# Kernel tuning notes

Measured on AMD Instinct MI355X. Metric: run time of the kernel, lower is better.

Reference implementation:

```python
import jax, jax.numpy as jnp
import numpy as np

B, S, H, NH, L = 2, 1024, 512, 8, 4
HD = H // NH
MLP = 4 * H
OUT = 128
SPARSITY = 0.8
EPS = 1e-5


def _pos_encoding(seq_len, d_model):
    pos = jnp.arange(seq_len, dtype=jnp.float32)[:, None]                     # [S,1]
    div = jnp.exp(jnp.arange(0, d_model, 2, dtype=jnp.float32) * (-np.log(10000.0) / d_model))
    ang = pos * div                                                            # [S,D/2]
    pe = jnp.stack([jnp.sin(ang), jnp.cos(ang)], axis=-1).reshape(seq_len, d_model)
    return pe[None]                                                            # [1,S,D]


def _layer_norm(x, g, b):
    m = jnp.mean(x, axis=-1, keepdims=True)
    v = jnp.mean(jnp.square(x - m), axis=-1, keepdims=True)
    return (x - m) * jax.lax.rsqrt(v + EPS) * g + b


def setup_inputs() -> dict:
    key = jax.random.key(0)
    ks = iter(jax.random.split(key, 16))
    w = lambda k, shp: jax.random.normal(k, shp, dtype=jnp.float32) * 0.02
    inp = {
        "x": jax.random.normal(next(ks), (B, S), dtype=jnp.float32),
        "in_w": w(next(ks), (1, H)), "in_b": jnp.zeros((H,), jnp.float32),
        "ln1_g": jnp.ones((L, H), jnp.float32), "ln1_b": jnp.zeros((L, H), jnp.float32),
        "qw": w(next(ks), (L, H, H)), "qb": jnp.zeros((L, H), jnp.float32),
        "kw": w(next(ks), (L, H, H)), "kb": jnp.zeros((L, H), jnp.float32),
        "vw": w(next(ks), (L, H, H)), "vb": jnp.zeros((L, H), jnp.float32),
        "ow": w(next(ks), (L, H, H)), "ob": jnp.zeros((L, H), jnp.float32),
        "ln2_g": jnp.ones((L, H), jnp.float32), "ln2_b": jnp.zeros((L, H), jnp.float32),
        "w1": w(next(ks), (L, H, MLP)), "b1": jnp.zeros((L, MLP), jnp.float32),
        "w2": w(next(ks), (L, MLP, H)), "b2": jnp.zeros((L, H), jnp.float32),
        "fn_g": jnp.ones((H,), jnp.float32), "fn_b": jnp.zeros((H,), jnp.float32),
        "out_w": w(next(ks), (H, OUT)), "out_b": jnp.zeros((OUT,), jnp.float32),
    }
    return inp


def _forward(x, in_w, in_b, ln1_g, ln1_b, qw, qb, kw, kb, vw, vb, ow, ob,
             ln2_g, ln2_b, w1, b1, w2, b2, fn_g, fn_b, out_w, out_b):
    seq_len = x.shape[1]
    k_top = max(1, int(seq_len * (1.0 - SPARSITY)))  # static
    scale = HD ** -0.5

    h = x[..., None] @ in_w + in_b                    # [B,S,H] (input_proj on [B,S,1])
    h = h + _pos_encoding(seq_len, H)

    layer_params = (ln1_g, ln1_b, qw, qb, kw, kb, vw, vb, ow, ob,
                    ln2_g, ln2_b, w1, b1, w2, b2)

    def block(h, p):
        (g1, bb1, Wq, bq, Wk, bk, Wv, bv, Wo, bo, g2, bb2, W1, B1, W2, B2) = p
        n = _layer_norm(h, g1, bb1)
        # project and split heads: [B,S,H] -> [B,NH,S,HD]
        def heads(W, b):
            y = n @ W + b
            return y.reshape(B, seq_len, NH, HD).transpose(0, 2, 1, 3)
        q, k, v = heads(Wq, bq), heads(Wk, bk), heads(Wv, bv)
        scores = jnp.einsum('bhqd,bhkd->bhqk', q, k) * scale
        # top-k sparsification: keep entries >= k-th largest per row (-inf elsewhere)
        kth = jax.lax.top_k(scores, k_top)[0][..., -1:]
        sparse = jnp.where(scores >= kth, scores, -jnp.inf)
        attn = jax.nn.softmax(sparse, axis=-1)
        o = jnp.einsum('bhqk,bhkd->bhqd', attn, v)
        o = o.transpose(0, 2, 1, 3).reshape(B, seq_len, H)
        h = h + (o @ Wo + bo)
        m = _layer_norm(h, g2, bb2)
        m = jax.nn.gelu(m @ W1 + B1, approximate=False) @ W2 + B2
        return h + m, attn

    h, attn_stack = jax.lax.scan(block, h, layer_params)
    out = _layer_norm(h, fn_g, fn_b) @ out_w + out_b  # [B,S,OUT]
    return out, attn_stack                            # attn_stack: [L,B,NH,S,S]


def reference(x, in_w, in_b, ln1_g, ln1_b, qw, qb, kw, kb, vw, vb, ow, ob,
              ln2_g, ln2_b, w1, b1, w2, b2, fn_g, fn_b, out_w, out_b):
    return _forward(x, in_w, in_b, ln1_g, ln1_b, qw, qb, kw, kb, vw, vb, ow, ob,
                    ln2_g, ln2_b, w1, b1, w2, b2, fn_g, fn_b, out_w, out_b)
```

## Files before the change

kernel.cpp:

```cpp
#include <hip/hip_runtime.h>
#include <math.h>

#define DEVINL __device__ __forceinline__

constexpr int S_   = 1024;
constexpr int H_   = 512;
constexpr int NH_  = 8;
constexpr int L_   = 4;
constexpr int HD_  = 64;
constexpr int MLP_ = 2048;
constexpr int OUT_ = 128;
constexpr int B_   = 2;
constexpr int BS_  = 2048;
constexpr int KTOP_ = 204;

typedef __bf16 bf16x8 __attribute__((ext_vector_type(8)));
typedef float f32x4 __attribute__((ext_vector_type(4)));

DEVINL unsigned short f2b(float f) {
  unsigned int u = __float_as_uint(f);
  unsigned int r = (u + 0x7fffu + ((u >> 16) & 1u)) >> 16;
  return (unsigned short)r;
}

__global__ __launch_bounds__(256) void transpose_conv_kernel(
    const float* __restrict__ src, unsigned short* __restrict__ dst, int R, int C)
{
  __shared__ float tile[32][33];
  const size_t base = (size_t)blockIdx.z * R * C;
  src += base; dst += base;
  const int c0 = blockIdx.x * 32;
  const int r0 = blockIdx.y * 32;
  const int tx = threadIdx.x & 31;
  const int ty = threadIdx.x >> 5;
#pragma unroll
  for (int j = 0; j < 4; j++)
    tile[ty + j * 8][tx] = src[(size_t)(r0 + ty + j * 8) * C + c0 + tx];
  __syncthreads();
#pragma unroll
  for (int j = 0; j < 4; j++)
    dst[(size_t)(c0 + ty + j * 8) * R + r0 + tx] = f2b(tile[tx][ty + j * 8]);
}

__global__ __launch_bounds__(256) void transpose_qkvo_kernel(
    const float* __restrict__ qw, const float* __restrict__ kw,
    const float* __restrict__ vw, const float* __restrict__ ow,
    unsigned short* __restrict__ qkv, unsigned short* __restrict__ ot)
{
  __shared__ float tile[32][33];
  const int z = blockIdx.z;
  const int which = z >> 2, l = z & 3;
  const float* src = (which == 0 ? qw : which == 1 ? kw : which == 2 ? vw : ow)
                     + (size_t)l * 512 * 512;
  unsigned short* dst = (which < 3)
      ? (qkv + (size_t)l * 1536 * 512 + (size_t)which * 512 * 512)
      : (ot + (size_t)l * 512 * 512);
  const int c0 = blockIdx.x * 32;
  const int r0 = blockIdx.y * 32;
  const int tx = threadIdx.x & 31;
  const int ty = threadIdx.x >> 5;
#pragma unroll
  for (int j = 0; j < 4; j++)
    tile[ty + j * 8][tx] = src[(size_t)(r0 + ty + j * 8) * 512 + c0 + tx];
  __syncthreads();
#pragma unroll
  for (int j = 0; j < 4; j++)
    dst[(size_t)(c0 + ty + j * 8) * 512 + r0 + tx] = f2b(tile[tx][ty + j * 8]);
}

__global__ __launch_bounds__(128) void input_pe_kernel(
    const float* __restrict__ x, const float* __restrict__ in_w,
    const float* __restrict__ in_b, float* __restrict__ h)
{
  const int row = blockIdx.x;
  const int s = row & (S_ - 1);
  const int c = threadIdx.x * 4;
  const float xv = x[row];
  const float4 wv = *(const float4*)(in_w + c);
  const float4 bv = *(const float4*)(in_b + c);
  const float* wp = (const float*)&wv;
  const float* bp = (const float*)&bv;
  float o[4];
#pragma unroll
  for (int j = 0; j < 4; j++) {
    const int cc = c + j;
    const float di = expf(-(float)(cc & ~1) * (9.210340371976184f / 512.0f));
    const float ang = (float)s * di;
    const float pe = (cc & 1) ? cosf(ang) : sinf(ang);
    o[j] = xv * wp[j] + bp[j] + pe;
  }
  *(float4*)(h + (size_t)row * H_ + c) = make_float4(o[0], o[1], o[2], o[3]);
}

__global__ __launch_bounds__(128) void ln_kernel(
    const float* __restrict__ hin, const float* __restrict__ g,
    const float* __restrict__ b, unsigned short* __restrict__ nout)
{
  const int row = blockIdx.x;
  const int t = threadIdx.x;
  const int wid = t >> 6, ln_ = t & 63;
  __shared__ float red[2];
  float4 v = ((const float4*)(hin + (size_t)row * H_))[t];
  float sm = v.x + v.y + v.z + v.w;
#pragma unroll
  for (int m = 1; m < 64; m <<= 1) sm += __shfl_xor(sm, m);
  if (ln_ == 0) red[wid] = sm;
  __syncthreads();
  const float mean = (red[0] + red[1]) * (1.0f / 512.0f);
  __syncthreads();
  const float dx = v.x - mean, dy = v.y - mean, dz = v.z - mean, dw = v.w - mean;
  float ss = dx * dx + dy * dy + dz * dz + dw * dw;
#pragma unroll
  for (int m = 1; m < 64; m <<= 1) ss += __shfl_xor(ss, m);
  if (ln_ == 0) red[wid] = ss;
  __syncthreads();
  const float var = (red[0] + red[1]) * (1.0f / 512.0f);
  const float rs = rsqrtf(var + 1e-5f);
  const float4 gv = ((const float4*)g)[t];
  const float4 bv = ((const float4*)b)[t];
  ushort4 o;
  o.x = f2b(dx * rs * gv.x + bv.x);
  o.y = f2b(dy * rs * gv.y + bv.y);
  o.z = f2b(dz * rs * gv.z + bv.z);
  o.w = f2b(dw * rs * gv.w + bv.w);
  ((ushort4*)(nout + (size_t)row * H_))[t] = o;
}

template <int EPI>
__global__ __launch_bounds__(256, 2) void gemm_kernel(
    const unsigned short* __restrict__ A, const unsigned short* __restrict__ Bt,
    const float* __restrict__ bias, void* __restrict__ Cout, int M, int N, int K,
    const float* __restrict__ bias2, const float* __restrict__ bias3,
    void* __restrict__ C2, void* __restrict__ C3)
{
  constexpr int LDK = 56;
  __shared__ unsigned short Alds[128 * LDK];
  __shared__ unsigned short Blds[128 * LDK];
  const int tid = threadIdx.x;
  const int w = tid >> 6, lane = tid & 63, lr = lane & 15, lg = lane >> 4;
  const int m0 = blockIdx.x * 128, n0 = blockIdx.y * 128;
  const int wm = (w >> 1) * 64, wn = (w & 1) * 64;

  const int e0 = tid * 8;
  const int r0 = e0 >> 5, c0 = e0 & 31;
  const unsigned short* Ap0 = A + (size_t)(m0 + r0) * K + c0;
  const unsigned short* Ap1 = Ap0 + (size_t)64 * K;
  const unsigned short* Bp0 = Bt + (size_t)(n0 + r0) * K + c0;
  const unsigned short* Bp1 = Bp0 + (size_t)64 * K;
  unsigned short* AL0 = Alds + r0 * LDK + c0;
  unsigned short* AL1 = AL0 + 64 * LDK;
  unsigned short* BL0 = Blds + r0 * LDK + c0;
  unsigned short* BL1 = BL0 + 64 * LDK;

  const f32x4 zero4 = {0.f, 0.f, 0.f, 0.f};
  f32x4 acc[4][4];
#pragma unroll
  for (int i = 0; i < 4; i++)
#pragma unroll
    for (int j = 0; j < 4; j++) acc[i][j] = zero4;

  for (int kt = 0; kt < K; kt += 32) {
    const int4 a0 = *(const int4*)(Ap0 + kt);
    const int4 a1 = *(const int4*)(Ap1 + kt);
    const int4 b0 = *(const int4*)(Bp0 + kt);
    const int4 b1 = *(const int4*)(Bp1 + kt);
    __syncthreads();
    *(int4*)AL0 = a0; *(int4*)AL1 = a1;
    *(int4*)BL0 = b0; *(int4*)BL1 = b1;
    __syncthreads();
    bf16x8 af[4], bfr[4];
#pragma unroll
    for (int mi = 0; mi < 4; mi++)
      af[mi] = *(const bf16x8*)(Alds + (wm + mi * 16 + lr) * LDK + lg * 8);
#pragma unroll
    for (int ni = 0; ni < 4; ni++)
      bfr[ni] = *(const bf16x8*)(Blds + (wn + ni * 16 + lr) * LDK + lg * 8);
#pragma unroll
    for (int mi = 0; mi < 4; mi++)
#pragma unroll
      for (int ni = 0; ni < 4; ni++)
        acc[mi][ni] = __builtin_amdgcn_mfma_f32_16x16x32_bf16(af[mi], bfr[ni], acc[mi][ni], 0, 0, 0);
  }

#pragma unroll
  for (int mi = 0; mi < 4; mi++) {
#pragma unroll
    for (int ni = 0; ni < 4; ni++) {
      const int col = n0 + wn + ni * 16 + lr;
      if constexpr (EPI == 5) {
        if (col < 512) {
          const float bs = bias[col];
#pragma unroll
          for (int r = 0; r < 4; r++) {
            const int row = m0 + wm + mi * 16 + lg * 4 + r;
            ((unsigned short*)Cout)[(size_t)row * 512 + col] =
                f2b((acc[mi][ni][r] + bs) * 0.125f);
          }
        } else if (col < 1024) {
          const float bs = bias2[col - 512];
#pragma unroll
          for (int r = 0; r < 4; r++) {
            const int row = m0 + wm + mi * 16 + lg * 4 + r;
            ((unsigned short*)C2)[(size_t)row * 512 + (col - 512)] =
                f2b(acc[mi][ni][r] + bs);
          }
        } else {
          const float bs = bias3[col - 1024];
          const int row0_ = m0 + wm + mi * 16 + lg * 4;
          const int bb = row0_ >> 10, ssi = row0_ & 1023;
          ushort4 pk;
          pk.x = f2b(acc[mi][ni][0] + bs);
          pk.y = f2b(acc[mi][ni][1] + bs);
          pk.z = f2b(acc[mi][ni][2] + bs);
          pk.w = f2b(acc[mi][ni][3] + bs);
          *(ushort4*)((unsigned short*)C3 + ((size_t)(bb * 512 + (col - 1024))) * 1024 + ssi) = pk;
        }
      } else {
        const float bs = bias[col];
#pragma unroll
        for (int r = 0; r < 4; r++) {
          const int row = m0 + wm + mi * 16 + lg * 4 + r;
          float val = acc[mi][ni][r] + bs;
          const size_t idx = (size_t)row * N + col;
          if constexpr (EPI == 1) {
            ((float*)Cout)[idx] += val;
          } else if constexpr (EPI == 2) {
            val = 0.5f * val * (1.0f + erff(val * 0.7071067811865475f));
            ((unsigned short*)Cout)[idx] = f2b(val);
          } else {
            ((float*)Cout)[idx] = val;
          }
        }
      }
    }
  }
}

__global__ __launch_bounds__(256, 2) void attn_fused_kernel(
    const unsigned short* __restrict__ qbf, const unsigned short* __restrict__ kbf,
    const unsigned short* __restrict__ vt, float* __restrict__ attnL,
    unsigned short* __restrict__ obf)
{
  constexpr int LDF = 1032;
  __shared__ float sc[16 * LDF];
  const int mblk = blockIdx.x, bnh = blockIdx.y;
  const int b = bnh >> 3, nh = bnh & 7;
  const int tid = threadIdx.x, w = tid >> 6, lane = tid & 63;
  const int lr = lane & 15, lg = lane >> 4;
  const int row0 = mblk * 16;

  const unsigned short* qbase = qbf + ((size_t)(b * S_ + row0)) * H_ + nh * HD_;
  const unsigned short* kbase = kbf + (size_t)(b * S_) * H_ + nh * HD_;

  const f32x4 zero4 = {0.f, 0.f, 0.f, 0.f};

  {
    f32x4 acc[16];
#pragma unroll
    for (int kt = 0; kt < 16; kt++) acc[kt] = zero4;
    bf16x8 qf[2];
    qf[0] = *(const bf16x8*)(qbase + (size_t)lr * H_ + lg * 8);
    qf[1] = *(const bf16x8*)(qbase + (size_t)lr * H_ + 32 + lg * 8);
    const int kw0 = w * 256;
#pragma unroll
    for (int kt = 0; kt < 16; kt++) {
      const unsigned short* kp = kbase + (size_t)(kw0 + kt * 16 + lr) * H_ + lg * 8;
      const bf16x8 kf0 = *(const bf16x8*)(kp);
      const bf16x8 kf1 = *(const bf16x8*)(kp + 32);
      acc[kt] = __builtin_amdgcn_mfma_f32_16x16x32_bf16(kf0, qf[0], acc[kt], 0, 0, 0);
      acc[kt] = __builtin_amdgcn_mfma_f32_16x16x32_bf16(kf1, qf[1], acc[kt], 0, 0, 0);
    }
#pragma unroll
    for (int kt = 0; kt < 16; kt++)
      *(f32x4*)(sc + (size_t)lr * LDF + kw0 + kt * 16 + lg * 4) = acc[kt];
  }
  __syncthreads();

#pragma unroll 1
  for (int rr = 0; rr < 4; rr++) {
    const int row = w * 4 + rr;
    float* rowp = sc + (size_t)row * LDF;
    float v[16];
#pragma unroll
    for (int j = 0; j < 8; j++) {
      const float2 t2 = *(const float2*)(rowp + 2 * lane + j * 128);
      v[2 * j] = t2.x; v[2 * j + 1] = t2.y;
    }
    unsigned int keys[16];
#pragma unroll
    for (int j = 0; j < 16; j++) {
      const unsigned int u = __float_as_uint(v[j]);
      keys[j] = (u & 0x80000000u) ? ~u : (u | 0x80000000u);
    }
    unsigned int prefix = 0u;
#pragma unroll 1
    for (int bit = 31; bit >= 0; bit--) {
      const unsigned int cand = prefix | (1u << bit);
      int cnt = 0;
#pragma unroll
      for (int j = 0; j < 16; j++)
        cnt += (int)__popcll(__ballot(keys[j] >= cand));
      if (cnt >= KTOP_) prefix = cand;
    }
    const unsigned int fb = (prefix & 0x80000000u) ? (prefix & 0x7fffffffu) : ~prefix;
    const float thresh = __uint_as_float(fb);

    float mx = v[0];
#pragma unroll
    for (int j = 1; j < 16; j++) mx = fmaxf(mx, v[j]);
#pragma unroll
    for (int m = 1; m < 64; m <<= 1) mx = fmaxf(mx, __shfl_xor(mx, m));
    float p[16];
    float ssum = 0.f;
#pragma unroll
    for (int j = 0; j < 16; j++) {
      const float e = expf(v[j] - mx);
      p[j] = (v[j] >= thresh) ? e : 0.f;
      ssum += p[j];
    }
#pragma unroll
    for (int m = 1; m < 64; m <<= 1) ssum += __shfl_xor(ssum, m);
    const float inv = 1.0f / ssum;
    float* outrow = attnL + (size_t)bnh * S_ * S_ + (size_t)(row0 + row) * S_;
    unsigned short* prow = (unsigned short*)rowp;
#pragma unroll
    for (int j = 0; j < 8; j++) {
      const float p0 = p[2 * j] * inv, p1 = p[2 * j + 1] * inv;
      *(float2*)(outrow + 2 * lane + j * 128) = make_float2(p0, p1);
      const unsigned int pk = ((unsigned int)f2b(p1) << 16) | (unsigned int)f2b(p0);
      *(unsigned int*)(prow + 2 * lane + j * 128) = pk;
    }
  }
  __syncthreads();

  const unsigned short* vb = vt + (size_t)(b * 512 + nh * HD_) * S_;
  f32x4 oacc[4];
#pragma unroll
  for (int ni = 0; ni < 4; ni++) oacc[ni] = zero4;
  const unsigned short* scu = (const unsigned short*)sc;
#pragma unroll
  for (int ks = 0; ks < 8; ks++) {
    const int k0 = w * 256 + ks * 32;
    const bf16x8 pf = *(const bf16x8*)(scu + (size_t)lr * (2 * LDF) + k0 + lg * 8);
    bf16x8 vfr[4];
#pragma unroll
    for (int ni = 0; ni < 4; ni++)
      vfr[ni] = *(const bf16x8*)(vb + (size_t)(ni * 16 + lr) * S_ + k0 + lg * 8);
#pragma unroll
    for (int ni = 0; ni < 4; ni++)
      oacc[ni] = __builtin_amdgcn_mfma_f32_16x16x32_bf16(pf, vfr[ni], oacc[ni], 0, 0, 0);
  }
  __syncthreads();
  float* red = sc + w * 1024;
#pragma unroll
  for (int ni = 0; ni < 4; ni++)
#pragma unroll
    for (int r = 0; r < 4; r++)
      red[(lg * 4 + r) * 64 + ni * 16 + lr] = oacc[ni][r];
  __syncthreads();
  {
    const int orow = tid >> 4, oc0 = (tid & 15) * 4;
    const float* rp = sc + orow * 64 + oc0;
    float4 s0 = *(const float4*)rp;
#pragma unroll
    for (int ww = 1; ww < 4; ww++) {
      const float4 a = *(const float4*)(rp + ww * 1024);
      s0.x += a.x; s0.y += a.y; s0.z += a.z; s0.w += a.w;
    }
    ushort4 o1;
    o1.x = f2b(s0.x); o1.y = f2b(s0.y); o1.z = f2b(s0.z); o1.w = f2b(s0.w);
    unsigned short* dst = obf + (size_t)(b * S_ + row0 + orow) * H_ + nh * HD_ + oc0;
    *(ushort4*)dst = o1;
  }
}

extern "C" void kernel_launch(void* const* d_in, const int* in_sizes, int n_in,
                              void* d_out, int out_size, void* d_ws, size_t ws_size,
                              hipStream_t stream)
{
  (void)in_sizes; (void)n_in; (void)out_size; (void)ws_size;
  const float* x     = (const float*)d_in[0];
  const float* in_w  = (const float*)d_in[1];
  const float* in_b  = (const float*)d_in[2];
  const float* ln1_g = (const float*)d_in[3];
  const float* ln1_b = (const float*)d_in[4];
  const float* qw    = (const float*)d_in[5];
  const float* qbias = (const float*)d_in[6];
  const float* kw    = (const float*)d_in[7];
  const float* kbias = (const float*)d_in[8];
  const float* vw    = (const float*)d_in[9];
  const float* vbias = (const float*)d_in[10];
  const float* ow    = (const float*)d_in[11];
  const float* obias = (const float*)d_in[12];
  const float* ln2_g = (const float*)d_in[13];
  const float* ln2_b = (const float*)d_in[14];
  const float* w1    = (const float*)d_in[15];
  const float* b1    = (const float*)d_in[16];
  const float* w2    = (const float*)d_in[17];
  const float* b2    = (const float*)d_in[18];
  const float* fn_g  = (const float*)d_in[19];
  const float* fn_b  = (const float*)d_in[20];
  const float* out_w = (const float*)d_in[21];
  const float* out_b = (const float*)d_in[22];

  char* ws = (char*)d_ws;
  size_t off = 0;
  auto alloc = [&](size_t bytes) -> void* {
    void* p = ws + off;
    off += (bytes + 255) & ~(size_t)255;
    return p;
  };
  float* h             = (float*)alloc((size_t)BS_ * H_ * 4);
  unsigned short* Wqkvt = (unsigned short*)alloc((size_t)L_ * 1536 * H_ * 2);
  unsigned short* Wot  = (unsigned short*)alloc((size_t)L_ * H_ * H_ * 2);
  unsigned short* W1t  = (unsigned short*)alloc((size_t)L_ * MLP_ * H_ * 2);
  unsigned short* W2t  = (unsigned short*)alloc((size_t)L_ * H_ * MLP_ * 2);
  unsigned short* OWt  = (unsigned short*)alloc((size_t)OUT_ * H_ * 2);
  unsigned short* nbf  = (unsigned short*)alloc((size_t)BS_ * H_ * 2);
  unsigned short* qbf  = (unsigned short*)alloc((size_t)BS_ * H_ * 2);
  unsigned short* kbf  = (unsigned short*)alloc((size_t)BS_ * H_ * 2);
  unsigned short* vtb  = (unsigned short*)alloc((size_t)B_ * 512 * S_ * 2);
  unsigned short* obf  = (unsigned short*)alloc((size_t)BS_ * H_ * 2);
  unsigned short* tbf  = (unsigned short*)alloc((size_t)BS_ * MLP_ * 2);

  float* attn_base = (float*)d_out + (size_t)BS_ * OUT_;

  const dim3 tb(256);
  transpose_qkvo_kernel<<<dim3(16, 16, 16), tb, 0, stream>>>(qw, kw, vw, ow, Wqkvt, Wot);
  transpose_conv_kernel<<<dim3(64, 16, 4), tb, 0, stream>>>(w1, W1t, H_, MLP_);
  transpose_conv_kernel<<<dim3(16, 64, 4), tb, 0, stream>>>(w2, W2t, MLP_, H_);
  transpose_conv_kernel<<<dim3(4, 16, 1),  tb, 0, stream>>>(out_w, OWt, H_, OUT_);

  input_pe_kernel<<<dim3(BS_), dim3(128), 0, stream>>>(x, in_w, in_b, h);

  for (int l = 0; l < L_; l++) {
    float* attnL = attn_base + (size_t)l * 16 * S_ * S_;
    ln_kernel<<<dim3(BS_), dim3(128), 0, stream>>>(h, ln1_g + l * H_, ln1_b + l * H_, nbf);
    gemm_kernel<5><<<dim3(16, 12), tb, 0, stream>>>(
        nbf, Wqkvt + (size_t)l * 1536 * H_, qbias + l * H_, qbf, BS_, 1536, H_,
        kbias + l * H_, vbias + l * H_, kbf, vtb);
    attn_fused_kernel<<<dim3(64, 16), tb, 0, stream>>>(qbf, kbf, vtb, attnL, obf);
    gemm_kernel<1><<<dim3(16, 4), tb, 0, stream>>>(
        obf, Wot + (size_t)l * H_ * H_, obias + l * H_, h, BS_, H_, H_,
        nullptr, nullptr, nullptr, nullptr);
    ln_kernel<<<dim3(BS_), dim3(128), 0, stream>>>(h, ln2_g + l * H_, ln2_b + l * H_, nbf);
    gemm_kernel<2><<<dim3(16, 16), tb, 0, stream>>>(
        nbf, W1t + (size_t)l * MLP_ * H_, b1 + l * MLP_, tbf, BS_, MLP_, H_,
        nullptr, nullptr, nullptr, nullptr);
    gemm_kernel<1><<<dim3(16, 4), tb, 0, stream>>>(
        tbf, W2t + (size_t)l * H_ * MLP_, b2 + l * H_, h, BS_, H_, MLP_,
        nullptr, nullptr, nullptr, nullptr);
  }

  ln_kernel<<<dim3(BS_), dim3(128), 0, stream>>>(h, fn_g, fn_b, nbf);
  gemm_kernel<3><<<dim3(16, 1), tb, 0, stream>>>(
      nbf, OWt, out_b, d_out, BS_, OUT_, H_,
      nullptr, nullptr, nullptr, nullptr);
}
```

Baseline: 1.194 ms.

## Split-K residual GEMMs with atomics and direct global-to-LDS loads

The output-projection and MLP-down GEMMs, which only launch 64 blocks, are split along K into 2 and 4 slices over blockIdx.z. Each slice atomically adds its partial result into the residual stream, and only slice 0 adds the bias. All GEMMs now stage tiles with global_load_lds straight into an unpadded 32-wide LDS layout instead of going through registers. The aim is better CU occupancy on the small GEMMs and less register staging, at the cost of atomic traffic, non-deterministic summation order, and possible LDS bank conflicts without padding.

```diff
diff --git a/kernel.cpp b/kernel.cpp
--- a/kernel.cpp
+++ b/kernel.cpp
@@ -21,6 +21,13 @@
   unsigned int u = __float_as_uint(f);
   unsigned int r = (u + 0x7fffu + ((u >> 16) & 1u)) >> 16;
   return (unsigned short)r;
+}
+
+DEVINL void gload16(const unsigned short* g, unsigned short* l) {
+  __builtin_amdgcn_global_load_lds(
+      (const __attribute__((address_space(1))) unsigned int*)g,
+      (__attribute__((address_space(3))) unsigned int*)l,
+      16, 0, 0);
 }
 
 __global__ __launch_bounds__(256) void transpose_conv_kernel(
@@ -129,28 +136,31 @@
 template <int EPI>
 __global__ __launch_bounds__(256, 2) void gemm_kernel(
     const unsigned short* __restrict__ A, const unsigned short* __restrict__ Bt,
-    const float* __restrict__ bias, void* __restrict__ Cout, int M, int N, int K,
+    const float* __restrict__ bias, void* __restrict__ Cout,
+    int M, int N, int Klen, int Kstride,
     const float* __restrict__ bias2, const float* __restrict__ bias3,
     void* __restrict__ C2, void* __restrict__ C3)
 {
-  constexpr int LDK = 56;
-  __shared__ unsigned short Alds[128 * LDK];
-  __shared__ unsigned short Blds[128 * LDK];
+  __shared__ unsigned short Alds[128 * 32];
+  __shared__ unsigned short Blds[128 * 32];
   const int tid = threadIdx.x;
   const int w = tid >> 6, lane = tid & 63, lr = lane & 15, lg = lane >> 4;
   const int m0 = blockIdx.x * 128, n0 = blockIdx.y * 128;
   const int wm = (w >> 1) * 64, wn = (w & 1) * 64;
 
-  const int e0 = tid * 8;
-  const int r0 = e0 >> 5, c0 = e0 & 31;
-  const unsigned short* Ap0 = A + (size_t)(m0 + r0) * K + c0;
-  const unsigned short* Ap1 = Ap0 + (size_t)64 * K;
-  const unsigned short* Bp0 = Bt + (size_t)(n0 + r0) * K + c0;
-  const unsigned short* Bp1 = Bp0 + (size_t)64 * K;
-  unsigned short* AL0 = Alds + r0 * LDK + c0;
-  unsigned short* AL1 = AL0 + 64 * LDK;
-  unsigned short* BL0 = Blds + r0 * LDK + c0;
-  unsigned short* BL1 = BL0 + 64 * LDK;
+  A  += (size_t)blockIdx.z * Klen;
+  Bt += (size_t)blockIdx.z * Klen;
+
+  const int srow = w * 32 + (lane >> 2);
+  const int scol = (lane & 3) * 8;
+  const unsigned short* Ag0 = A + (size_t)(m0 + srow) * Kstride + scol;
+  const unsigned short* Ag1 = A + (size_t)(m0 + srow + 16) * Kstride + scol;
+  const unsigned short* Bg0 = Bt + (size_t)(n0 + srow) * Kstride + scol;
+  const unsigned short* Bg1 = Bt + (size_t)(n0 + srow + 16) * Kstride + scol;
+  unsigned short* Al0 = Alds + (w * 32) * 32;
+  unsigned short* Al1 = Alds + (w * 32 + 16) * 32;
+  unsigned short* Bl0 = Blds + (w * 32) * 32;
+  unsigned short* Bl1 = Blds + (w * 32 + 16) * 32;
 
   const f32x4 zero4 = {0.f, 0.f, 0.f, 0.f};
   f32x4 acc[4][4];
@@ -159,22 +169,20 @@
 #pragma unroll
     for (int j = 0; j < 4; j++) acc[i][j] = zero4;
 
-  for (int kt = 0; kt < K; kt += 32) {
-    const int4 a0 = *(const int4*)(Ap0 + kt);
-    const int4 a1 = *(const int4*)(Ap1 + kt);
-    const int4 b0 = *(const int4*)(Bp0 + kt);
-    const int4 b1 = *(const int4*)(Bp1 + kt);
+  for (int kt = 0; kt < Klen; kt += 32) {
     __syncthreads();
-    *(int4*)AL0 = a0; *(int4*)AL1 = a1;
-    *(int4*)BL0 = b0; *(int4*)BL1 = b1;
+    gload16(Ag0 + kt, Al0);
+    gload16(Ag1 + kt, Al1);
+    gload16(Bg0 + kt, Bl0);
+    gload16(Bg1 + kt, Bl1);
     __syncthreads();
     bf16x8 af[4], bfr[4];
 #pragma unroll
     for (int mi = 0; mi < 4; mi++)
-      af[mi] = *(const bf16x8*)(Alds + (wm + mi * 16 + lr) * LDK + lg * 8);
+      af[mi] = *(const bf16x8*)(Alds + (wm + mi * 16 + lr) * 32 + lg * 8);
 #pragma unroll
     for (int ni = 0; ni < 4; ni++)
-      bfr[ni] = *(const bf16x8*)(Blds + (wn + ni * 16 + lr) * LDK + lg * 8);
+      bfr[ni] = *(const bf16x8*)(Blds + (wn + ni * 16 + lr) * 32 + lg * 8);
 #pragma unroll
     for (int mi = 0; mi < 4; mi++)
 #pragma unroll
@@ -215,6 +223,13 @@
           pk.w = f2b(acc[mi][ni][3] + bs);
           *(ushort4*)((unsigned short*)C3 + ((size_t)(bb * 512 + (col - 1024))) * 1024 + ssi) = pk;
         }
+      } else if constexpr (EPI == 6) {
+        const float bs = (blockIdx.z == 0) ? bias[col] : 0.f;
+#pragma unroll
+        for (int r = 0; r < 4; r++) {
+          const int row = m0 + wm + mi * 16 + lg * 4 + r;
+          atomicAdd(&((float*)Cout)[(size_t)row * N + col], acc[mi][ni][r] + bs);
+        }
       } else {
         const float bs = bias[col];
 #pragma unroll
@@ -222,9 +237,7 @@
           const int row = m0 + wm + mi * 16 + lg * 4 + r;
           float val = acc[mi][ni][r] + bs;
           const size_t idx = (size_t)row * N + col;
-          if constexpr (EPI == 1) {
-            ((float*)Cout)[idx] += val;
-          } else if constexpr (EPI == 2) {
+          if constexpr (EPI == 2) {
             val = 0.5f * val * (1.0f + erff(val * 0.7071067811865475f));
             ((unsigned short*)Cout)[idx] = f2b(val);
           } else {
@@ -437,23 +450,23 @@
     float* attnL = attn_base + (size_t)l * 16 * S_ * S_;
     ln_kernel<<<dim3(BS_), dim3(128), 0, stream>>>(h, ln1_g + l * H_, ln1_b + l * H_, nbf);
     gemm_kernel<5><<<dim3(16, 12), tb, 0, stream>>>(
-        nbf, Wqkvt + (size_t)l * 1536 * H_, qbias + l * H_, qbf, BS_, 1536, H_,
+        nbf, Wqkvt + (size_t)l * 1536 * H_, qbias + l * H_, qbf, BS_, 1536, H_, H_,
         kbias + l * H_, vbias + l * H_, kbf, vtb);
     attn_fused_kernel<<<dim3(64, 16), tb, 0, stream>>>(qbf, kbf, vtb, attnL, obf);
-    gemm_kernel<1><<<dim3(16, 4), tb, 0, stream>>>(
-        obf, Wot + (size_t)l * H_ * H_, obias + l * H_, h, BS_, H_, H_,
+    gemm_kernel<6><<<dim3(16, 4, 2), tb, 0, stream>>>(
+        obf, Wot + (size_t)l * H_ * H_, obias + l * H_, h, BS_, H_, 256, H_,
         nullptr, nullptr, nullptr, nullptr);
     ln_kernel<<<dim3(BS_), dim3(128), 0, stream>>>(h, ln2_g + l * H_, ln2_b + l * H_, nbf);
     gemm_kernel<2><<<dim3(16, 16), tb, 0, stream>>>(
-        nbf, W1t + (size_t)l * MLP_ * H_, b1 + l * MLP_, tbf, BS_, MLP_, H_,
+        nbf, W1t + (size_t)l * MLP_ * H_, b1 + l * MLP_, tbf, BS_, MLP_, H_, H_,
         nullptr, nullptr, nullptr, nullptr);
-    gemm_kernel<1><<<dim3(16, 4), tb, 0, stream>>>(
-        tbf, W2t + (size_t)l * H_ * MLP_, b2 + l * H_, h, BS_, H_, MLP_,
+    gemm_kernel<6><<<dim3(16, 4, 4), tb, 0, stream>>>(
+        tbf, W2t + (size_t)l * H_ * MLP_, b2 + l * H_, h, BS_, H_, 512, MLP_,
         nullptr, nullptr, nullptr, nullptr);
   }
 
   ln_kernel<<<dim3(BS_), dim3(128), 0, stream>>>(h, fn_g, fn_b, nbf);
   gemm_kernel<3><<<dim3(16, 1), tb, 0, stream>>>(
-      nbf, OWt, out_b, d_out, BS_, OUT_, H_,
+      nbf, OWt, out_b, d_out, BS_, OUT_, H_, H_,
       nullptr, nullptr, nullptr, nullptr);
 }
```

Result: faster. 1.037 ms (-13.1%).
